# Kernel tuning notes

Hardware: AMD Instinct MI355X
Metric: run time of the kernel (lower is better)

## Reference

```python
import jax, jax.numpy as jnp
import numpy as np

NC = 80            # number of classes (COCO)
NM = 32            # mask coefficients (YOLOv5-seg)
D = 4 + 1 + NC + NM
N_ANCHORS = 100800  # 1280x1280 input, strides 8/16/32, 3 anchors
CONF_THRES = 0.25
IOU_THRES = 0.45
MAX_DET = 300
TOPK = 4096        # fixed pre-NMS candidate budget (jit-compatible stand-in for boolean filter)


def setup_inputs() -> dict:
    key = jax.random.key(0)
    x = jax.random.uniform(key, (1, N_ANCHORS, D), dtype=jnp.float32)
    return {"x": x}


def _pairwise_iou(boxes):
    # boxes: [K, 4] in (y1, x1, y2, x2)
    y1, x1, y2, x2 = boxes[:, 0], boxes[:, 1], boxes[:, 2], boxes[:, 3]
    area = (y2 - y1) * (x2 - x1)
    iy1 = jnp.maximum(y1[:, None], y1[None, :])
    ix1 = jnp.maximum(x1[:, None], x1[None, :])
    iy2 = jnp.minimum(y2[:, None], y2[None, :])
    ix2 = jnp.minimum(x2[:, None], x2[None, :])
    inter = jnp.clip(iy2 - iy1, 0.0) * jnp.clip(ix2 - ix1, 0.0)
    union = area[:, None] + area[None, :] - inter
    return inter / jnp.maximum(union, 1e-9)


def reference(x):
    p = x[0]                                   # [N, D] (loop returns after first image)
    obj = p[:, 4]
    valid = obj > CONF_THRES                   # candidates = obj score > conf_thres
    cls_scores = p[:, 5:5 + NC] * obj[:, None] # scores = cls * obj
    scores = jnp.max(cls_scores, axis=1)
    classes = jnp.argmax(cls_scores, axis=1).astype(x.dtype)
    # xywh (center) -> yxyx
    xc, yc, w, h = p[:, 0], p[:, 1], p[:, 2], p[:, 3]
    yxyx = jnp.stack([yc - h * 0.5, xc - w * 0.5, yc + h * 0.5, xc + w * 0.5], axis=1)
    masks = p[:, 5 + NC:]                      # [N, NM]
    # replace torch's boolean-filter gather with fixed-size top-K over masked scores
    scores_m = jnp.where(valid, scores, -1.0)
    top_s, top_i = jax.lax.top_k(scores_m, TOPK)   # sorted desc, as torchvision nms requires
    b = yxyx[top_i]                            # [K, 4]
    keep0 = top_s > -0.5                       # only real candidates
    iou = _pairwise_iou(b)                     # [K, K]
    j_idx = jnp.arange(TOPK)

    def body(i, keep):
        sup = keep[i] & (iou[i] > IOU_THRES) & (j_idx > i)
        return keep & ~sup

    keep = jax.lax.fori_loop(0, TOPK, body, keep0)
    # pad/select top MAX_DET surviving detections (score -1.0 marks padding)
    sel_s = jnp.where(keep, top_s, -1.0)
    out_s, out_i = jax.lax.top_k(sel_s, MAX_DET)
    gi = top_i[out_i]
    return (yxyx[gi][None], classes[gi][None], out_s[None], masks[gi][None])
```

## Files before the change

kernel.cpp:

```cpp
#include <hip/hip_runtime.h>


#define AS1 __attribute__((address_space(1)))
#define AS3 __attribute__((address_space(3)))

constexpr int    N_ANCH = 100800;
constexpr int    DIMV   = 117;
constexpr int    TOPKN  = 4096;
constexpr int    MAXDET = 300;
constexpr int    KCAP   = 12288;
constexpr int    NBUCK  = 16384;
constexpr int    NSLICE = 8;

constexpr int PACK_TOT = 133120;

constexpr size_t WS_SLICES = 0;
constexpr size_t WS_SCORES = WS_SLICES + (size_t)NSLICE * NBUCK * 4;
constexpr size_t WS_CLS    = WS_SCORES + (size_t)N_ANCH * 4;
constexpr size_t WS_SEL    = WS_CLS    + (size_t)N_ANCH * 4;
constexpr size_t WS_KEYS   = WS_SEL    + 256;
constexpr size_t WS_RANK   = WS_KEYS   + (size_t)KCAP * 8;
constexpr size_t WS_SIDX   = WS_RANK   + (size_t)KCAP * 4;
constexpr size_t WS_SSC    = WS_SIDX   + 4096ull * 4;
constexpr size_t WS_BOXES  = WS_SSC    + 4096ull * 4;
constexpr size_t WS_MASKP  = WS_BOXES  + 4096ull * 16;
constexpr size_t WS_DIAG   = WS_MASKP  + (size_t)PACK_TOT * 8 + 4096;
constexpr size_t WS_OUTI   = WS_DIAG   + 4096ull * 8;
constexpr size_t WS_OUTS   = WS_OUTI   + 1280;

__global__ void zero_kernel(unsigned* __restrict__ slices, int* __restrict__ sel) {
    int i = blockIdx.x * 256 + threadIdx.x;
    if (i < NSLICE * NBUCK) slices[i] = 0u;
    if (i < 64)             sel[i]    = 0;
}

constexpr int SROWS = 64;
__global__ void score_kernel(const float* __restrict__ x, float* __restrict__ scores,
                             int* __restrict__ cls, unsigned* __restrict__ slices) {
    __shared__ float sx[SROWS * DIMV];
    int block0 = blockIdx.x * SROWS;
    const float4* src = (const float4*)(x + (size_t)block0 * DIMV);
    float4* dst = (float4*)sx;
    constexpr int NV4 = SROWS * DIMV / 4;
    for (int i = threadIdx.x; i < NV4; i += 128) dst[i] = src[i];
    __syncthreads();
    int row  = threadIdx.x >> 1;
    int half = threadIdx.x & 1;
    const float* rp = sx + row * DIMV;
    float obj = rp[4];
    const float* cp = rp + 5 + half * 40;
    float best = -1.0f;
    int   bc   = half * 40;
#pragma unroll 8
    for (int c = 0; c < 40; ++c) {
        float s = __fmul_rn(cp[c], obj);
        if (s > best) { best = s; bc = half * 40 + c; }
    }
    float so = __shfl_xor(best, 1);
    int   co = __shfl_xor(bc, 1);
    if (half == 0) {
        if (so > best) { best = so; bc = co; }
        int a = block0 + row;
        bool valid = obj > 0.25f;
        scores[a] = valid ? best : -1.0f;
        cls[a]    = bc;
        if (valid) {
            unsigned b = __float_as_uint(best) >> 16;
            atomicAdd(&slices[(blockIdx.x & (NSLICE - 1)) * NBUCK + b], 1u);
        }
    }
}

__global__ void select_kernel(const unsigned* __restrict__ slices, int* sel) {
    __shared__ unsigned sv[1024];
    int t = threadIdx.x;
    int base = NBUCK - 16 * (t + 1);
    unsigned hb[16];
#pragma unroll
    for (int k = 0; k < 16; ++k) hb[k] = 0u;
    for (int s = 0; s < NSLICE; ++s) {
        const uint4* hp = (const uint4*)(slices + (size_t)s * NBUCK + base);
#pragma unroll
        for (int q = 0; q < 4; ++q) {
            uint4 v = hp[q];
            hb[q * 4 + 0] += v.x; hb[q * 4 + 1] += v.y;
            hb[q * 4 + 2] += v.z; hb[q * 4 + 3] += v.w;
        }
    }
    unsigned own = 0;
#pragma unroll
    for (int k = 0; k < 16; ++k) own += hb[k];
    sv[t] = own;
    __syncthreads();
    for (int off = 1; off < 1024; off <<= 1) {
        unsigned v = (t >= off) ? sv[t - off] : 0u;
        __syncthreads();
        sv[t] += v;
        __syncthreads();
    }
    unsigned incl = sv[t];
    unsigned before = incl - own;
    if (before < (unsigned)TOPKN && incl >= (unsigned)TOPKN) {
        unsigned running = before;
        for (int k = 15; k >= 0; --k) {
            running += hb[k];
            if (running >= (unsigned)TOPKN) {
                sel[0] = base + k;
                sel[1] = (int)(running - hb[k]);
                break;
            }
        }
    }
}

__global__ void compact_kernel(const float* __restrict__ scores, int* sel,
                               unsigned long long* __restrict__ keys,
                               int* __restrict__ rank) {
    int a = blockIdx.x * blockDim.x + threadIdx.x;
    if (a < KCAP) rank[a] = 0;
    if (a >= N_ANCH) return;
    float s = scores[a];
    if (s < 0.0f) return;
    unsigned bits = __float_as_uint(s);
    if ((int)(bits >> 16) < sel[0]) return;
    int pos = atomicAdd(&sel[2], 1);
    if (pos < KCAP) keys[pos] = ((unsigned long long)bits << 32) | (unsigned)(~a);
}

constexpr int NCOLP = 8;
__global__ void rank_kernel(const unsigned long long* __restrict__ keys,
                            const int* __restrict__ sel, int* __restrict__ rank) {
    __shared__ unsigned long long tile[2048];
    int n = sel[2]; if (n > KCAP) n = KCAP;
    if (blockIdx.x * 256 >= n) return;
    int t0 = blockIdx.y * 2048;
    if (t0 >= n) return;
    int i = blockIdx.x * 256 + threadIdx.x;
    unsigned long long myKey = (i < n) ? keys[i] : 0ull;
    int m = n - t0; if (m > 2048) m = 2048;
    for (int j = threadIdx.x; j < m; j += 256) tile[j] = keys[t0 + j];
    __syncthreads();
    int cnt = 0;
    int j = 0;
    for (; j + 3 < m; j += 4) {
        cnt += (tile[j]     > myKey);
        cnt += (tile[j + 1] > myKey);
        cnt += (tile[j + 2] > myKey);
        cnt += (tile[j + 3] > myKey);
    }
    for (; j < m; ++j) cnt += (tile[j] > myKey);
    if (i < n && cnt) atomicAdd(&rank[i], cnt);
}

__global__ void scatter_kernel(const float* __restrict__ x,
                               const unsigned long long* __restrict__ keys,
                               const int* __restrict__ sel, const int* __restrict__ rank,
                               int* __restrict__ sidx, float* __restrict__ sscore,
                               float* __restrict__ boxes) {
    int n = sel[2]; if (n > KCAP) n = KCAP;
    int i = blockIdx.x * 256 + threadIdx.x;
    if (i >= n) return;
    int r = rank[i];
    if (r >= TOPKN) return;
    unsigned long long k = keys[i];
    int a = (int)(~(unsigned)(k & 0xFFFFFFFFull));
    sidx[r]   = a;
    sscore[r] = __uint_as_float((unsigned)(k >> 32));
    const float* p = x + (size_t)a * DIMV;
    float xc = p[0], yc = p[1], w = p[2], h = p[3];
    float hw = __fmul_rn(w, 0.5f);
    float hh = __fmul_rn(h, 0.5f);
    boxes[r * 4 + 0] = __fsub_rn(yc, hh);
    boxes[r * 4 + 1] = __fsub_rn(xc, hw);
    boxes[r * 4 + 2] = __fadd_rn(yc, hh);
    boxes[r * 4 + 3] = __fadd_rn(xc, hw);
}

__global__ void iou_mask_kernel(const float* __restrict__ boxes,
                                unsigned long long* __restrict__ maskp,
                                unsigned long long* __restrict__ diag) {
    int colT = blockIdx.x, rowT = blockIdx.y;
    if (colT < rowT) return;
    int t = threadIdx.x;
    __shared__ float cb[64][5];
    const float4* bp = (const float4*)boxes;
    int cj = colT * 64 + t;
    {
        float4 c = bp[cj];
        cb[t][0] = c.x; cb[t][1] = c.y; cb[t][2] = c.z; cb[t][3] = c.w;
        cb[t][4] = __fmul_rn(__fsub_rn(c.z, c.x), __fsub_rn(c.w, c.y));
    }
    __syncthreads();
    int r = rowT * 64 + t;
    float4 rv = bp[r];
    float ry1 = rv.x, rx1 = rv.y, ry2 = rv.z, rx2 = rv.w;
    float rarea = __fmul_rn(__fsub_rn(ry2, ry1), __fsub_rn(rx2, rx1));
    unsigned long long bitsw = 0ull;
#pragma unroll 8
    for (int j = 0; j < 64; ++j) {
        float iy1 = fmaxf(ry1, cb[j][0]);
        float ix1 = fmaxf(rx1, cb[j][1]);
        float iy2 = fminf(ry2, cb[j][2]);
        float ix2 = fminf(rx2, cb[j][3]);
        float ih = fmaxf(__fsub_rn(iy2, iy1), 0.0f);
        float iw = fmaxf(__fsub_rn(ix2, ix1), 0.0f);
        float inter = __fmul_rn(ih, iw);
        float uni = __fsub_rn(__fadd_rn(rarea, cb[j][4]), inter);
        float iou = __fdiv_rn(inter, fmaxf(uni, 1e-9f));
        if (iou > 0.45f && (colT * 64 + j) > r) bitsw |= (1ull << j);
    }
    int pb = 64 * (64 * rowT - (rowT * (rowT - 1)) / 2);
    maskp[pb + t * (64 - rowT) + (colT - rowT)] = bitsw;
    if (colT == rowT) diag[(rowT << 6) + t] = bitsw;
}

__device__ __forceinline__ unsigned long long readlane64(unsigned long long v, int l) {
    unsigned lo = (unsigned)__builtin_amdgcn_readlane((int)(unsigned)(v & 0xFFFFFFFFull), l);
    unsigned hi = (unsigned)__builtin_amdgcn_readlane((int)(unsigned)(v >> 32), l);
    return ((unsigned long long)hi << 32) | lo;
}

__global__ void __launch_bounds__(64, 1)
nms_scan_kernel(const unsigned long long* __restrict__ maskp,
                const unsigned long long* __restrict__ diagG,
                const float* __restrict__ sscore,
                int* __restrict__ outIdx, float* __restrict__ outScore) {
    int lane = threadIdx.x;
    unsigned long long remv = 0ull;
    __shared__ __align__(16) unsigned long long tile[2 * 4096];
    __shared__ __align__(16) unsigned long long diagLds[4096];
    __shared__ int keepArr[MAXDET];
    __shared__ unsigned long long remvFinal[64];
    int count = 0;

    auto issueBatch = [&](int w) {
        if (w >= 64) return;
        int L = (65 - w) >> 1;
        const char* gbase = (const char*)maskp +
                            (size_t)(64 * (64 * w - (w * (w - 1)) / 2)) * 8 +
                            (size_t)lane * 16;
        char* lbase = (char*)tile + (size_t)(w & 1) * 32768;
        for (int i = 0; i < L; ++i) {
            __builtin_amdgcn_global_load_lds(
                (AS1 const unsigned*)(gbase + (size_t)i * 1024),
                (AS3 unsigned*)(lbase + (size_t)i * 1024), 16, 0, 0);
        }
    };

    {
        const char* gb = (const char*)diagG + (size_t)lane * 16;
        char* lb = (char*)diagLds;
#pragma unroll
        for (int i = 0; i < 32; ++i) {
            __builtin_amdgcn_global_load_lds(
                (AS1 const unsigned*)(gb + (size_t)i * 1024),
                (AS3 unsigned*)(lb + (size_t)i * 1024), 16, 0, 0);
        }
    }
    issueBatch(0);

#define VW(n) asm volatile("s_waitcnt vmcnt(" #n ")" ::: "memory")

    for (int w = 0; w < 64 && count < MAXDET; ++w) {
        issueBatch(w + 1);
        unsigned long long cand = __shfl(~remv, w);
        if (!cand) continue;
        int p = (w < 63) ? ((64 - w) >> 1) : 0;
        switch (p) {
            case 32: VW(32); break; case 31: VW(31); break; case 30: VW(30); break;
            case 29: VW(29); break; case 28: VW(28); break; case 27: VW(27); break;
            case 26: VW(26); break; case 25: VW(25); break; case 24: VW(24); break;
            case 23: VW(23); break; case 22: VW(22); break; case 21: VW(21); break;
            case 20: VW(20); break; case 19: VW(19); break; case 18: VW(18); break;
            case 17: VW(17); break; case 16: VW(16); break; case 15: VW(15); break;
            case 14: VW(14); break; case 13: VW(13); break; case 12: VW(12); break;
            case 11: VW(11); break; case 10: VW(10); break; case  9: VW(9);  break;
            case  8: VW(8);  break; case  7: VW(7);  break; case  6: VW(6);  break;
            case  5: VW(5);  break; case  4: VW(4);  break; case  3: VW(3);  break;
            case  2: VW(2);  break; case  1: VW(1);  break; default: VW(0);  break;
        }
        unsigned long long diagv = diagLds[(w << 6) | lane];
        unsigned long long alive = cand;
        unsigned long long keptM = 0ull;
        while (alive && count < MAXDET) {
            int b = (int)__builtin_ctzll(alive);
            unsigned long long db = readlane64(diagv, b);
            if (lane == 0) keepArr[count] = (w << 6) + b;
            count++;
            keptM |= (1ull << b);
            alive &= ~(db | (1ull << b));
        }
        const unsigned long long* trow = tile + (size_t)(w & 1) * 4096;
        int stride = 64 - w;
        int rel = lane - w;
        while (keptM) {
            int bs[4]; unsigned long long t2 = keptM; int g = 0;
#pragma unroll
            for (int t = 0; t < 4; ++t) {
                bs[t] = t2 ? (int)__builtin_ctzll(t2) : 0;
                if (t2) { t2 &= t2 - 1; g = t + 1; }
            }
            unsigned long long vs[4];
#pragma unroll
            for (int t = 0; t < 4; ++t)
                vs[t] = (rel >= 0) ? trow[bs[t] * stride + rel] : 0ull;
#pragma unroll
            for (int t = 0; t < 4; ++t)
                if (t < g) remv |= vs[t];
            keptM = t2;
        }
    }
    __syncthreads();
    remvFinal[lane] = remv;
    __syncthreads();
    int K = count;
    for (int k = lane; k < K; k += 64) {
        int s = keepArr[k];
        outIdx[k] = s;
        outScore[k] = sscore[s];
    }
    if (K < MAXDET && lane == 0) {
        int filled = K;
        for (int w = 0; w < 64 && filled < MAXDET; ++w) {
            unsigned long long word = remvFinal[w];
            while (word && filled < MAXDET) {
                int b = (int)__builtin_ctzll(word);
                word &= word - 1;
                outIdx[filled] = (w << 6) + b;
                outScore[filled] = -1.0f;
                filled++;
            }
        }
    }
}

__global__ void write_out_kernel(const float* __restrict__ x, const int* __restrict__ sidx,
                                 const int* __restrict__ cls, const float* __restrict__ boxes,
                                 const int* __restrict__ outIdx, const float* __restrict__ outScore,
                                 float* __restrict__ out) {
    int o = blockIdx.x;
    int t = threadIdx.x;
    int s = outIdx[o];
    int a = sidx[s];
    if (t < 32) {
        out[1800 + o * 32 + t] = x[(size_t)a * DIMV + 85 + t];
    } else if (t < 36) {
        out[o * 4 + (t - 32)] = boxes[s * 4 + (t - 32)];
    } else if (t == 36) {
        out[1200 + o] = (float)cls[a];
    } else if (t == 37) {
        out[1500 + o] = outScore[o];
    }
}

extern "C" void kernel_launch(void* const* d_in, const int* in_sizes, int n_in,
                              void* d_out, int out_size, void* d_ws, size_t ws_size,
                              hipStream_t stream) {
    const float* x = (const float*)d_in[0];
    char* ws = (char*)d_ws;
    unsigned*            slices = (unsigned*)(ws + WS_SLICES);
    float*               scores = (float*)(ws + WS_SCORES);
    int*                 cls    = (int*)(ws + WS_CLS);
    int*                 sel    = (int*)(ws + WS_SEL);
    unsigned long long*  keys   = (unsigned long long*)(ws + WS_KEYS);
    int*                 rank   = (int*)(ws + WS_RANK);
    int*                 sidx   = (int*)(ws + WS_SIDX);
    float*               sscore = (float*)(ws + WS_SSC);
    float*               boxes  = (float*)(ws + WS_BOXES);
    unsigned long long*  maskp  = (unsigned long long*)(ws + WS_MASKP);
    unsigned long long*  diag   = (unsigned long long*)(ws + WS_DIAG);
    int*                 outIdx = (int*)(ws + WS_OUTI);
    float*               outSc  = (float*)(ws + WS_OUTS);

    zero_kernel<<<(NSLICE * NBUCK) / 256, 256, 0, stream>>>(slices, sel);
    score_kernel<<<N_ANCH / SROWS, 128, 0, stream>>>(x, scores, cls, slices);
    select_kernel<<<1, 1024, 0, stream>>>(slices, sel);
    compact_kernel<<<(N_ANCH + 255) / 256, 256, 0, stream>>>(scores, sel, keys, rank);
    dim3 rg(KCAP / 256, NCOLP);
    rank_kernel<<<rg, 256, 0, stream>>>(keys, sel, rank);
    scatter_kernel<<<KCAP / 256, 256, 0, stream>>>(x, keys, sel, rank, sidx, sscore, boxes);
    dim3 mg(64, 64);
    iou_mask_kernel<<<mg, 64, 0, stream>>>(boxes, maskp, diag);
    nms_scan_kernel<<<1, 64, 0, stream>>>(maskp, diag, sscore, outIdx, outSc);
    write_out_kernel<<<MAXDET, 64, 0, stream>>>(x, sidx, cls, boxes, outIdx, outSc, (float*)d_out);
}
```

Measured before the change: 247.3 us.

## Fuse select+compact, deepen NMS tile prefetch, drop separate diag buffer

Merges the bucket-select and compaction kernels into one single-block kernel, so a launch is removed but all 100800 scores are now scanned by only 1024 threads. The NMS scan kernel now prefetches three mask row-tiles ahead into a 4-slot LDS ring instead of one. It reads the diagonal block from the packed tile, which removes the separate diag buffer and its preload. Histogram slices double to 16 to cut atomic contention in score_kernel. The single-block compaction could become a serial bottleneck.

New measurement: 262.2 us. 6.0% more time.

```diff
diff --git a/kernel.cpp b/kernel.cpp
--- a/kernel.cpp
+++ b/kernel.cpp
@@ -10,7 +10,7 @@
 constexpr int    MAXDET = 300;
 constexpr int    KCAP   = 12288;
 constexpr int    NBUCK  = 16384;
-constexpr int    NSLICE = 8;
+constexpr int    NSLICE = 16;
 
 constexpr int PACK_TOT = 133120;
 
@@ -24,8 +24,7 @@
 constexpr size_t WS_SSC    = WS_SIDX   + 4096ull * 4;
 constexpr size_t WS_BOXES  = WS_SSC    + 4096ull * 4;
 constexpr size_t WS_MASKP  = WS_BOXES  + 4096ull * 16;
-constexpr size_t WS_DIAG   = WS_MASKP  + (size_t)PACK_TOT * 8 + 4096;
-constexpr size_t WS_OUTI   = WS_DIAG   + 4096ull * 8;
+constexpr size_t WS_OUTI   = WS_MASKP  + (size_t)PACK_TOT * 8 + 4096;
 constexpr size_t WS_OUTS   = WS_OUTI   + 1280;
 
 __global__ void zero_kernel(unsigned* __restrict__ slices, int* __restrict__ sel) {
@@ -71,8 +70,14 @@
     }
 }
 
-__global__ void select_kernel(const unsigned* __restrict__ slices, int* sel) {
+__global__ void select_compact_kernel(const unsigned* __restrict__ slices,
+                                      const float* __restrict__ scores,
+                                      int* __restrict__ sel,
+                                      unsigned long long* __restrict__ keys,
+                                      int* __restrict__ rank) {
     __shared__ unsigned sv[1024];
+    __shared__ int selB;
+    __shared__ int nctr;
     int t = threadIdx.x;
     int base = NBUCK - 16 * (t + 1);
     unsigned hb[16];
@@ -91,6 +96,7 @@
 #pragma unroll
     for (int k = 0; k < 16; ++k) own += hb[k];
     sv[t] = own;
+    if (t == 0) { selB = 0; nctr = 0; }
     __syncthreads();
     for (int off = 1; off < 1024; off <<= 1) {
         unsigned v = (t >= off) ? sv[t - off] : 0u;
@@ -104,27 +110,22 @@
         unsigned running = before;
         for (int k = 15; k >= 0; --k) {
             running += hb[k];
-            if (running >= (unsigned)TOPKN) {
-                sel[0] = base + k;
-                sel[1] = (int)(running - hb[k]);
-                break;
-            }
-        }
-    }
-}
-
-__global__ void compact_kernel(const float* __restrict__ scores, int* sel,
-                               unsigned long long* __restrict__ keys,
-                               int* __restrict__ rank) {
-    int a = blockIdx.x * blockDim.x + threadIdx.x;
-    if (a < KCAP) rank[a] = 0;
-    if (a >= N_ANCH) return;
-    float s = scores[a];
-    if (s < 0.0f) return;
-    unsigned bits = __float_as_uint(s);
-    if ((int)(bits >> 16) < sel[0]) return;
-    int pos = atomicAdd(&sel[2], 1);
-    if (pos < KCAP) keys[pos] = ((unsigned long long)bits << 32) | (unsigned)(~a);
+            if (running >= (unsigned)TOPKN) { selB = base + k; break; }
+        }
+    }
+    __syncthreads();
+    int B = selB;
+    for (int a = t; a < KCAP; a += 1024) rank[a] = 0;
+    for (int a = t; a < N_ANCH; a += 1024) {
+        float s = scores[a];
+        if (s < 0.0f) continue;
+        unsigned bits = __float_as_uint(s);
+        if ((int)(bits >> 16) < B) continue;
+        int pos = atomicAdd(&nctr, 1);
+        if (pos < KCAP) keys[pos] = ((unsigned long long)bits << 32) | (unsigned)(~a);
+    }
+    __syncthreads();
+    if (t == 0) sel[2] = (nctr > KCAP) ? KCAP : nctr;
 }
 
 constexpr int NCOLP = 8;
@@ -177,8 +178,7 @@
 }
 
 __global__ void iou_mask_kernel(const float* __restrict__ boxes,
-                                unsigned long long* __restrict__ maskp,
-                                unsigned long long* __restrict__ diag) {
+                                unsigned long long* __restrict__ maskp) {
     int colT = blockIdx.x, rowT = blockIdx.y;
     if (colT < rowT) return;
     int t = threadIdx.x;
@@ -211,7 +211,6 @@
     }
     int pb = 64 * (64 * rowT - (rowT * (rowT - 1)) / 2);
     maskp[pb + t * (64 - rowT) + (colT - rowT)] = bitsw;
-    if (colT == rowT) diag[(rowT << 6) + t] = bitsw;
 }
 
 __device__ __forceinline__ unsigned long long readlane64(unsigned long long v, int l) {
@@ -222,13 +221,11 @@
 
 __global__ void __launch_bounds__(64, 1)
 nms_scan_kernel(const unsigned long long* __restrict__ maskp,
-                const unsigned long long* __restrict__ diagG,
                 const float* __restrict__ sscore,
                 int* __restrict__ outIdx, float* __restrict__ outScore) {
     int lane = threadIdx.x;
     unsigned long long remv = 0ull;
-    __shared__ __align__(16) unsigned long long tile[2 * 4096];
-    __shared__ __align__(16) unsigned long long diagLds[4096];
+    __shared__ __align__(16) unsigned long long tile[4 * 4096];
     __shared__ int keepArr[MAXDET];
     __shared__ unsigned long long remvFinal[64];
     int count = 0;
@@ -239,7 +236,7 @@
         const char* gbase = (const char*)maskp +
                             (size_t)(64 * (64 * w - (w * (w - 1)) / 2)) * 8 +
                             (size_t)lane * 16;
-        char* lbase = (char*)tile + (size_t)(w & 1) * 32768;
+        char* lbase = (char*)tile + (size_t)(w & 3) * 32768;
         for (int i = 0; i < L; ++i) {
             __builtin_amdgcn_global_load_lds(
                 (AS1 const unsigned*)(gbase + (size_t)i * 1024),
@@ -247,39 +244,42 @@
         }
     };
 
-    {
-        const char* gb = (const char*)diagG + (size_t)lane * 16;
-        char* lb = (char*)diagLds;
-#pragma unroll
-        for (int i = 0; i < 32; ++i) {
-            __builtin_amdgcn_global_load_lds(
-                (AS1 const unsigned*)(gb + (size_t)i * 1024),
-                (AS3 unsigned*)(lb + (size_t)i * 1024), 16, 0, 0);
-        }
-    }
-    issueBatch(0);
+    issueBatch(0); issueBatch(1); issueBatch(2);
 
 #define VW(n) asm volatile("s_waitcnt vmcnt(" #n ")" ::: "memory")
 
     for (int w = 0; w < 64 && count < MAXDET; ++w) {
-        issueBatch(w + 1);
-        unsigned long long cand = __shfl(~remv, w);
+        issueBatch(w + 3);
+        unsigned long long cand = ~readlane64(remv, w);
         if (!cand) continue;
-        int p = (w < 63) ? ((64 - w) >> 1) : 0;
-        switch (p) {
-            case 32: VW(32); break; case 31: VW(31); break; case 30: VW(30); break;
-            case 29: VW(29); break; case 28: VW(28); break; case 27: VW(27); break;
-            case 26: VW(26); break; case 25: VW(25); break; case 24: VW(24); break;
-            case 23: VW(23); break; case 22: VW(22); break; case 21: VW(21); break;
-            case 20: VW(20); break; case 19: VW(19); break; case 18: VW(18); break;
-            case 17: VW(17); break; case 16: VW(16); break; case 15: VW(15); break;
-            case 14: VW(14); break; case 13: VW(13); break; case 12: VW(12); break;
-            case 11: VW(11); break; case 10: VW(10); break; case  9: VW(9);  break;
-            case  8: VW(8);  break; case  7: VW(7);  break; case  6: VW(6);  break;
-            case  5: VW(5);  break; case  4: VW(4);  break; case  3: VW(3);  break;
-            case  2: VW(2);  break; case  1: VW(1);  break; default: VW(0);  break;
-        }
-        unsigned long long diagv = diagLds[(w << 6) | lane];
+        int P = ((w + 1 < 64) ? ((64 - w) >> 1) : 0)
+              + ((w + 2 < 64) ? ((63 - w) >> 1) : 0)
+              + ((w + 3 < 64) ? ((62 - w) >> 1) : 0);
+        if (P < 63) {
+            switch (P >> 1) {
+                case  0: VW(0);  break; case  1: VW(2);  break;
+                case  2: VW(4);  break; case  3: VW(6);  break;
+                case  4: VW(8);  break; case  5: VW(10); break;
+                case  6: VW(12); break; case  7: VW(14); break;
+                case  8: VW(16); break; case  9: VW(18); break;
+                case 10: VW(20); break; case 11: VW(22); break;
+                case 12: VW(24); break; case 13: VW(26); break;
+                case 14: VW(28); break; case 15: VW(30); break;
+                case 16: VW(32); break; case 17: VW(34); break;
+                case 18: VW(36); break; case 19: VW(38); break;
+                case 20: VW(40); break; case 21: VW(42); break;
+                case 22: VW(44); break; case 23: VW(46); break;
+                case 24: VW(48); break; case 25: VW(50); break;
+                case 26: VW(52); break; case 27: VW(54); break;
+                case 28: VW(56); break; case 29: VW(58); break;
+                case 30: VW(60); break; default: VW(62); break;
+            }
+        } else {
+            asm volatile("" ::: "memory");
+        }
+        const unsigned long long* trow = tile + (size_t)(w & 3) * 4096;
+        int stride = 64 - w;
+        unsigned long long diagv = trow[(size_t)lane * stride];
         unsigned long long alive = cand;
         unsigned long long keptM = 0ull;
         while (alive && count < MAXDET) {
@@ -290,8 +290,6 @@
             keptM |= (1ull << b);
             alive &= ~(db | (1ull << b));
         }
-        const unsigned long long* trow = tile + (size_t)(w & 1) * 4096;
-        int stride = 64 - w;
         int rel = lane - w;
         while (keptM) {
             int bs[4]; unsigned long long t2 = keptM; int g = 0;
@@ -368,19 +366,17 @@
     float*               sscore = (float*)(ws + WS_SSC);
     float*               boxes  = (float*)(ws + WS_BOXES);
     unsigned long long*  maskp  = (unsigned long long*)(ws + WS_MASKP);
-    unsigned long long*  diag   = (unsigned long long*)(ws + WS_DIAG);
     int*                 outIdx = (int*)(ws + WS_OUTI);
     float*               outSc  = (float*)(ws + WS_OUTS);
 
-    zero_kernel<<<(NSLICE * NBUCK) / 256, 256, 0, stream>>>(slices, sel);
+    zero_kernel<<<(NSLICE * NBUCK + 255) / 256, 256, 0, stream>>>(slices, sel);
     score_kernel<<<N_ANCH / SROWS, 128, 0, stream>>>(x, scores, cls, slices);
-    select_kernel<<<1, 1024, 0, stream>>>(slices, sel);
-    compact_kernel<<<(N_ANCH + 255) / 256, 256, 0, stream>>>(scores, sel, keys, rank);
+    select_compact_kernel<<<1, 1024, 0, stream>>>(slices, scores, sel, keys, rank);
     dim3 rg(KCAP / 256, NCOLP);
     rank_kernel<<<rg, 256, 0, stream>>>(keys, sel, rank);
     scatter_kernel<<<KCAP / 256, 256, 0, stream>>>(x, keys, sel, rank, sidx, sscore, boxes);
     dim3 mg(64, 64);
-    iou_mask_kernel<<<mg, 64, 0, stream>>>(boxes, maskp, diag);
-    nms_scan_kernel<<<1, 64, 0, stream>>>(maskp, diag, sscore, outIdx, outSc);
+    iou_mask_kernel<<<mg, 64, 0, stream>>>(boxes, maskp);
+    nms_scan_kernel<<<1, 64, 0, stream>>>(maskp, sscore, outIdx, outSc);
     write_out_kernel<<<MAXDET, 64, 0, stream>>>(x, sidx, cls, boxes, outIdx, outSc, (float*)d_out);
 }
```

## Deepen NMS scan prefetch to four LDS slots and split histogram reduction

Applied to the files above, without the earlier changes.

The NMS scan now prefetches mask-row batches three steps ahead into a four-slot LDS ring instead of double-buffering, and waits on a vmcnt that accounts for the outstanding batches. This is meant to hide global-to-LDS latency in the serial single-wave scan. Separately, the histogram slices grow from 8 to 16 to reduce atomic contention in the score kernel, and a new multi-block kernel reduces them so the single-block select kernel reads only one histogram. keepArr and remvFinal now reuse LDS regions to fit the larger buffer. The trade-off is one extra kernel launch and more zeroing work.

Measured after the change: 223.6 us. 9.6% less time.

```diff
diff --git a/kernel.cpp b/kernel.cpp
--- a/kernel.cpp
+++ b/kernel.cpp
@@ -10,11 +10,12 @@
 constexpr int    MAXDET = 300;
 constexpr int    KCAP   = 12288;
 constexpr int    NBUCK  = 16384;
-constexpr int    NSLICE = 8;
+constexpr int    NSLICE = 16;
 
 constexpr int PACK_TOT = 133120;
 
-constexpr size_t WS_SLICES = 0;
+constexpr size_t WS_HIST   = 0;
+constexpr size_t WS_SLICES = WS_HIST   + 65536;
 constexpr size_t WS_SCORES = WS_SLICES + (size_t)NSLICE * NBUCK * 4;
 constexpr size_t WS_CLS    = WS_SCORES + (size_t)N_ANCH * 4;
 constexpr size_t WS_SEL    = WS_CLS    + (size_t)N_ANCH * 4;
@@ -71,25 +72,29 @@
     }
 }
 
-__global__ void select_kernel(const unsigned* __restrict__ slices, int* sel) {
+__global__ void reduce_hist_kernel(const unsigned* __restrict__ slices,
+                                   unsigned* __restrict__ hist) {
+    int b = blockIdx.x * 256 + threadIdx.x;
+    unsigned s = 0;
+#pragma unroll
+    for (int k = 0; k < NSLICE; ++k) s += slices[(size_t)k * NBUCK + b];
+    hist[b] = s;
+}
+
+__global__ void select_kernel(const unsigned* __restrict__ hist, int* sel) {
     __shared__ unsigned sv[1024];
     int t = threadIdx.x;
     int base = NBUCK - 16 * (t + 1);
+    const uint4* hp = (const uint4*)(hist + base);
     unsigned hb[16];
-#pragma unroll
-    for (int k = 0; k < 16; ++k) hb[k] = 0u;
-    for (int s = 0; s < NSLICE; ++s) {
-        const uint4* hp = (const uint4*)(slices + (size_t)s * NBUCK + base);
-#pragma unroll
-        for (int q = 0; q < 4; ++q) {
-            uint4 v = hp[q];
-            hb[q * 4 + 0] += v.x; hb[q * 4 + 1] += v.y;
-            hb[q * 4 + 2] += v.z; hb[q * 4 + 3] += v.w;
-        }
-    }
     unsigned own = 0;
 #pragma unroll
-    for (int k = 0; k < 16; ++k) own += hb[k];
+    for (int q = 0; q < 4; ++q) {
+        uint4 v = hp[q];
+        hb[q * 4 + 0] = v.x; hb[q * 4 + 1] = v.y;
+        hb[q * 4 + 2] = v.z; hb[q * 4 + 3] = v.w;
+        own += v.x + v.y + v.z + v.w;
+    }
     sv[t] = own;
     __syncthreads();
     for (int off = 1; off < 1024; off <<= 1) {
@@ -227,10 +232,9 @@
                 int* __restrict__ outIdx, float* __restrict__ outScore) {
     int lane = threadIdx.x;
     unsigned long long remv = 0ull;
-    __shared__ __align__(16) unsigned long long tile[2 * 4096];
-    __shared__ __align__(16) unsigned long long diagLds[4096];
-    __shared__ int keepArr[MAXDET];
-    __shared__ unsigned long long remvFinal[64];
+    __shared__ __align__(16) unsigned long long ldsAll[20224];
+    constexpr int slotW[4] = {0, 4096, 8192, 12160};
+    unsigned long long* diagLds = ldsAll + 16128;
     int count = 0;
 
     auto issueBatch = [&](int w) {
@@ -239,7 +243,7 @@
         const char* gbase = (const char*)maskp +
                             (size_t)(64 * (64 * w - (w * (w - 1)) / 2)) * 8 +
                             (size_t)lane * 16;
-        char* lbase = (char*)tile + (size_t)(w & 1) * 32768;
+        char* lbase = (char*)(ldsAll + slotW[w & 3]);
         for (int i = 0; i < L; ++i) {
             __builtin_amdgcn_global_load_lds(
                 (AS1 const unsigned*)(gbase + (size_t)i * 1024),
@@ -257,31 +261,45 @@
                 (AS3 unsigned*)(lb + (size_t)i * 1024), 16, 0, 0);
         }
     }
-    issueBatch(0);
+    issueBatch(0); issueBatch(1); issueBatch(2);
 
 #define VW(n) asm volatile("s_waitcnt vmcnt(" #n ")" ::: "memory")
 
     for (int w = 0; w < 64 && count < MAXDET; ++w) {
-        issueBatch(w + 1);
-        unsigned long long cand = __shfl(~remv, w);
+        issueBatch(w + 3);
+        unsigned long long cand = ~readlane64(remv, w);
         if (!cand) continue;
-        int p = (w < 63) ? ((64 - w) >> 1) : 0;
-        switch (p) {
-            case 32: VW(32); break; case 31: VW(31); break; case 30: VW(30); break;
-            case 29: VW(29); break; case 28: VW(28); break; case 27: VW(27); break;
-            case 26: VW(26); break; case 25: VW(25); break; case 24: VW(24); break;
-            case 23: VW(23); break; case 22: VW(22); break; case 21: VW(21); break;
-            case 20: VW(20); break; case 19: VW(19); break; case 18: VW(18); break;
-            case 17: VW(17); break; case 16: VW(16); break; case 15: VW(15); break;
-            case 14: VW(14); break; case 13: VW(13); break; case 12: VW(12); break;
-            case 11: VW(11); break; case 10: VW(10); break; case  9: VW(9);  break;
-            case  8: VW(8);  break; case  7: VW(7);  break; case  6: VW(6);  break;
-            case  5: VW(5);  break; case  4: VW(4);  break; case  3: VW(3);  break;
-            case  2: VW(2);  break; case  1: VW(1);  break; default: VW(0);  break;
-        }
+        int P = ((w + 1 < 64) ? ((64 - w) >> 1) : 0)
+              + ((w + 2 < 64) ? ((63 - w) >> 1) : 0)
+              + ((w + 3 < 64) ? ((62 - w) >> 1) : 0);
+        if (P < 63) {
+            switch (P >> 1) {
+                case  0: VW(0);  break; case  1: VW(2);  break;
+                case  2: VW(4);  break; case  3: VW(6);  break;
+                case  4: VW(8);  break; case  5: VW(10); break;
+                case  6: VW(12); break; case  7: VW(14); break;
+                case  8: VW(16); break; case  9: VW(18); break;
+                case 10: VW(20); break; case 11: VW(22); break;
+                case 12: VW(24); break; case 13: VW(26); break;
+                case 14: VW(28); break; case 15: VW(30); break;
+                case 16: VW(32); break; case 17: VW(34); break;
+                case 18: VW(36); break; case 19: VW(38); break;
+                case 20: VW(40); break; case 21: VW(42); break;
+                case 22: VW(44); break; case 23: VW(46); break;
+                case 24: VW(48); break; case 25: VW(50); break;
+                case 26: VW(52); break; case 27: VW(54); break;
+                case 28: VW(56); break; case 29: VW(58); break;
+                case 30: VW(60); break; default: VW(62); break;
+            }
+        } else {
+            asm volatile("" ::: "memory");
+        }
+        const unsigned long long* trow = ldsAll + slotW[w & 3];
+        int stride = 64 - w;
         unsigned long long diagv = diagLds[(w << 6) | lane];
         unsigned long long alive = cand;
         unsigned long long keptM = 0ull;
+        int* keepArr = (int*)diagLds;
         while (alive && count < MAXDET) {
             int b = (int)__builtin_ctzll(alive);
             unsigned long long db = readlane64(diagv, b);
@@ -290,8 +308,6 @@
             keptM |= (1ull << b);
             alive &= ~(db | (1ull << b));
         }
-        const unsigned long long* trow = tile + (size_t)(w & 1) * 4096;
-        int stride = 64 - w;
         int rel = lane - w;
         while (keptM) {
             int bs[4]; unsigned long long t2 = keptM; int g = 0;
@@ -311,9 +327,11 @@
         }
     }
     __syncthreads();
+    unsigned long long* remvFinal = ldsAll;
     remvFinal[lane] = remv;
     __syncthreads();
     int K = count;
+    int* keepArr = (int*)diagLds;
     for (int k = lane; k < K; k += 64) {
         int s = keepArr[k];
         outIdx[k] = s;
@@ -358,6 +376,7 @@
                               hipStream_t stream) {
     const float* x = (const float*)d_in[0];
     char* ws = (char*)d_ws;
+    unsigned*            hist   = (unsigned*)(ws + WS_HIST);
     unsigned*            slices = (unsigned*)(ws + WS_SLICES);
     float*               scores = (float*)(ws + WS_SCORES);
     int*                 cls    = (int*)(ws + WS_CLS);
@@ -372,9 +391,10 @@
     int*                 outIdx = (int*)(ws + WS_OUTI);
     float*               outSc  = (float*)(ws + WS_OUTS);
 
-    zero_kernel<<<(NSLICE * NBUCK) / 256, 256, 0, stream>>>(slices, sel);
+    zero_kernel<<<(NSLICE * NBUCK + 255) / 256, 256, 0, stream>>>(slices, sel);
     score_kernel<<<N_ANCH / SROWS, 128, 0, stream>>>(x, scores, cls, slices);
-    select_kernel<<<1, 1024, 0, stream>>>(slices, sel);
+    reduce_hist_kernel<<<NBUCK / 256, 256, 0, stream>>>(slices, hist);
+    select_kernel<<<1, 1024, 0, stream>>>(hist, sel);
     compact_kernel<<<(N_ANCH + 255) / 256, 256, 0, stream>>>(scores, sel, keys, rank);
     dim3 rg(KCAP / 256, NCOLP);
     rank_kernel<<<rg, 256, 0, stream>>>(keys, sel, rank);
```
